# Performance work log

Hardware: AMD Instinct MI355X
Metric: run time of the kernel (lower is better)

The kernel has to match this reference:

```python
import jax, jax.numpy as jnp
import numpy as np

B, S, E, H, DK = 2, 2048, 2048, 16, 128


def _make_freq_pos_enc(dim, max_seq_len):
    # matches torch freq_pos_enc: interleaved repeat '(f r)' with r=2
    inv_freq = 1.0 / (10000.0 ** (jnp.arange(0, dim, 2, dtype=jnp.float32) / dim))
    pos = jnp.arange(max_seq_len, dtype=jnp.float32)
    pe = pos[:, None] * inv_freq[None, :]          # [S, dim/2]
    return jnp.repeat(pe, 2, axis=-1)              # [S, dim], interleaved


def setup_inputs() -> dict:
    key = jax.random.key(0)
    ks = jax.random.split(key, 5)
    sc = 1.0 / np.sqrt(E)
    return {
        "x": jax.random.normal(ks[0], (B, S, E), jnp.float32),
        "wq": jax.random.normal(ks[1], (H * DK, E), jnp.float32) * sc,
        "wk": jax.random.normal(ks[2], (H * DK, E), jnp.float32) * sc,
        "wv": jax.random.normal(ks[3], (H * DK, E), jnp.float32) * sc,
        "wo": jax.random.normal(ks[4], (E, H * DK), jnp.float32) * sc,
        "freq_pos_enc": _make_freq_pos_enc(DK, S),
        "num_heads": H,
        "d_k": DK,
    }


def rotate_half(u):
    # interleaved pairs: (d r) with r=2 -> (-u2, u1) interleaved back
    shp = u.shape
    u = u.reshape(shp[:-1] + (shp[-1] // 2, 2))
    u1, u2 = u[..., 0], u[..., 1]
    return jnp.stack((-u2, u1), axis=-1).reshape(shp)


def reference(x, wq, wk, wv, wo, freq_pos_enc, num_heads, d_k):
    b, s, _ = x.shape

    def proj(w):  # [B,S,E] @ [E, H*DK] -> [B,H,S,DK]
        return (x @ w.T).reshape(b, s, num_heads, d_k).transpose(0, 2, 1, 3)

    q, k, v = proj(wq), proj(wk), proj(wv)

    pe = freq_pos_enc[:s]                           # [S, DK]
    cos, sin = jnp.cos(pe), jnp.sin(pe)
    rot = lambda u: u * cos + rotate_half(u) * sin  # broadcast over [B,H]
    q, k = rot(q), rot(k)

    scale = 1.0 / jnp.sqrt(jnp.asarray(d_k, x.dtype))
    scores = jnp.einsum('bhqd,bhkd->bhqk', q, k) * scale
    causal = jnp.tril(jnp.ones((s, s), bool))
    scores = jnp.where(causal, scores, jnp.finfo(scores.dtype).min)
    attn = jnp.einsum('bhqk,bhkd->bhqd', jax.nn.softmax(scores, axis=-1), v)

    out = attn.transpose(0, 2, 1, 3).reshape(b, s, num_heads * d_k)
    return out @ wo.T
```

## Files before the change

kernel.cpp:

```cpp
#include <hip/hip_runtime.h>
#include <hip/hip_bf16.h>

typedef __attribute__((ext_vector_type(8))) short bf16x8;
typedef __attribute__((ext_vector_type(4))) float f32x4;
typedef unsigned short u16;
typedef unsigned int u32;

#define B_ 2
#define S_ 2048
#define E_ 2048
#define H_ 16
#define DK_ 128
#define SCALE_ 0.08838834764831845f
#define THR_RAW_ 90.5f

#define MFMA16(a,b,c) __builtin_amdgcn_mfma_f32_16x16x32_bf16((a),(b),(c),0,0,0)
#define GLD16(g, l) __builtin_amdgcn_global_load_lds((const __attribute__((address_space(1))) void*)(g), (__attribute__((address_space(3))) void*)(l), 16, 0, 0)

__device__ __forceinline__ float b2f(short s) {
    u32 u = ((u32)(u16)s) << 16;
    float f; __builtin_memcpy(&f, &u, 4); return f;
}

__global__ void cast_f32_bf16(const float* __restrict__ in, __hip_bfloat16* __restrict__ out, int n4) {
    int i = blockIdx.x * blockDim.x + threadIdx.x;
    if (i >= n4) return;
    float4 v = ((const float4*)in)[i];
    __hip_bfloat16 ob[4] = {__float2bfloat16(v.x), __float2bfloat16(v.y),
                            __float2bfloat16(v.z), __float2bfloat16(v.w)};
    ushort4 u; __builtin_memcpy(&u, ob, 8);
    ((ushort4*)out)[i] = u;
}

__global__ void cast_w4(const float* __restrict__ w0, const float* __restrict__ w1,
                        const float* __restrict__ w2, const float* __restrict__ w3,
                        __hip_bfloat16* __restrict__ o0, __hip_bfloat16* __restrict__ o1,
                        __hip_bfloat16* __restrict__ o2, __hip_bfloat16* __restrict__ o3,
                        int n4) {
    int i = blockIdx.x * blockDim.x + threadIdx.x;
    if (i >= n4) return;
    const float* in = blockIdx.y == 0 ? w0 : blockIdx.y == 1 ? w1 : blockIdx.y == 2 ? w2 : w3;
    __hip_bfloat16* out = blockIdx.y == 0 ? o0 : blockIdx.y == 1 ? o1 : blockIdx.y == 2 ? o2 : o3;
    float4 v = ((const float4*)in)[i];
    __hip_bfloat16 ob[4] = {__float2bfloat16(v.x), __float2bfloat16(v.y),
                            __float2bfloat16(v.z), __float2bfloat16(v.w)};
    ushort4 u; __builtin_memcpy(&u, ob, 8);
    ((ushort4*)out)[i] = u;
}

__global__ void trig_table(const float* __restrict__ pe, float* __restrict__ ct,
                           float* __restrict__ st) {
    int t = blockIdx.x * blockDim.x + threadIdx.x;
    int s = t >> 6, d2 = t & 63;
    float ang = pe[(size_t)s * DK_ + 2 * d2];
    ct[t] = cosf(ang);
    st[t] = sinf(ang);
}


#define ST_B(BUF, Q, KB) do { \
    int row_ = (Q) * 64 + (tid >> 3); \
    int gc_ = ((tid & 7) * 16) ^ ((row_ & 7) << 4); \
    GLD16(Wb + (size_t)(n0 + row_) * K2 + (KB) + gc_, (char*)Bs[BUF] + (Q) * 8192 + tid * 16); \
} while (0)

#define ST_A(BUF, Q, KB) do { \
    int row_ = (Q) * 64 + (tid >> 3); \
    int gc_ = ((tid & 7) * 16) ^ ((row_ & 7) << 4); \
    GLD16(Ab + (size_t)(m0 + row_) * K2 + (KB) + gc_, (char*)As[BUF] + (Q) * 8192 + tid * 16); \
} while (0)

#define WAIT_MFMA_ENTER() do { \
    __builtin_amdgcn_s_barrier(); \
    asm volatile("s_waitcnt lgkmcnt(0)" ::: "memory"); \
    __builtin_amdgcn_sched_barrier(0); \
    __builtin_amdgcn_s_setprio(1); \
} while (0)

__global__ __launch_bounds__(512, 2)
void gemm_qkv8(const __hip_bfloat16* __restrict__ X,
               const __hip_bfloat16* __restrict__ Wcat,
               __hip_bfloat16* __restrict__ Qo, __hip_bfloat16* __restrict__ Ko,
               __hip_bfloat16* __restrict__ Vo,
               const float* __restrict__ CT, const float* __restrict__ ST)
{
    __shared__ __align__(16) __hip_bfloat16 As[2][256 * 64];
    __shared__ __align__(16) __hip_bfloat16 Bs[2][192 * 64];
    const int tid = threadIdx.x, lane = tid & 63, wid = tid >> 6;
    const int wm = wid >> 2, wn = wid & 3;
    const int g = lane >> 4, c = lane & 15;
    const int raw = blockIdx.x;
    const int wg = (raw & 7) * 64 + (raw >> 3);
    const int mtile = wg & 15, ntile = wg >> 4;
    const int m0 = mtile * 256, n0 = ntile * 192;
    const long K2 = E_ * 2;
    const char* Ab = (const char*)X;
    const char* Wb = (const char*)Wcat;

    f32x4 acc[8][3];
    #pragma unroll
    for (int i = 0; i < 8; ++i)
        #pragma unroll
        for (int j = 0; j < 3; ++j) acc[i][j] = f32x4{0.f, 0.f, 0.f, 0.f};

    bf16x8 af[4][2], b01[2][2], b2[2];

    ST_B(0, 0, 0); ST_B(0, 1, 0); ST_B(0, 2, 0);
    ST_A(0, 0, 0); ST_A(0, 2, 0);
    ST_A(0, 1, 0); ST_A(0, 3, 0);
    asm volatile("s_waitcnt vmcnt(2)" ::: "memory");
    __builtin_amdgcn_s_barrier();

    #pragma unroll 1
    for (int t = 0; t < 32; ++t) {
        const int buf = t & 1;
        const long kb1 = (long)(t + 1) * 128;
        const char* Ac = (const char*)As[buf];
        const char* Bc = (const char*)Bs[buf];

        #pragma unroll
        for (int i = 0; i < 4; ++i) {
            int ar = wm * 128 + i * 16 + c;
            const char* ab = Ac + ar * 128;
            af[i][0] = *(const bf16x8*)(ab + ((g * 16) ^ ((ar & 7) << 4)));
            af[i][1] = *(const bf16x8*)(ab + ((64 + g * 16) ^ ((ar & 7) << 4)));
        }
        #pragma unroll
        for (int nj = 0; nj < 2; ++nj) {
            int br = wn * 48 + nj * 16 + c;
            const char* bb = Bc + br * 128;
            b01[nj][0] = *(const bf16x8*)(bb + ((g * 16) ^ ((br & 7) << 4)));
            b01[nj][1] = *(const bf16x8*)(bb + ((64 + g * 16) ^ ((br & 7) << 4)));
        }
        if (t < 31) { ST_B(buf ^ 1, 0, kb1); ST_B(buf ^ 1, 1, kb1); ST_B(buf ^ 1, 2, kb1); }
        WAIT_MFMA_ENTER();
        #pragma unroll
        for (int i = 0; i < 4; ++i)
            #pragma unroll
            for (int nj = 0; nj < 2; ++nj)
                #pragma unroll
                for (int k = 0; k < 2; ++k)
                    acc[i][nj] = MFMA16(af[i][k], b01[nj][k], acc[i][nj]);
        __builtin_amdgcn_s_setprio(0);
        __builtin_amdgcn_s_barrier();

        {
            int br = wn * 48 + 32 + c;
            const char* bb = Bc + br * 128;
            b2[0] = *(const bf16x8*)(bb + ((g * 16) ^ ((br & 7) << 4)));
            b2[1] = *(const bf16x8*)(bb + ((64 + g * 16) ^ ((br & 7) << 4)));
        }
        if (t < 31) { ST_A(buf ^ 1, 0, kb1); ST_A(buf ^ 1, 2, kb1); }
        WAIT_MFMA_ENTER();
        #pragma unroll
        for (int i = 0; i < 4; ++i)
            #pragma unroll
            for (int k = 0; k < 2; ++k)
                acc[i][2] = MFMA16(af[i][k], b2[k], acc[i][2]);
        __builtin_amdgcn_s_setprio(0);
        if (t < 31) { asm volatile("s_waitcnt vmcnt(5)" ::: "memory"); }
        else        { asm volatile("s_waitcnt vmcnt(0)" ::: "memory"); }
        __builtin_amdgcn_s_barrier();

        #pragma unroll
        for (int i = 0; i < 4; ++i) {
            int ar = wm * 128 + 64 + i * 16 + c;
            const char* ab = Ac + ar * 128;
            af[i][0] = *(const bf16x8*)(ab + ((g * 16) ^ ((ar & 7) << 4)));
            af[i][1] = *(const bf16x8*)(ab + ((64 + g * 16) ^ ((ar & 7) << 4)));
        }
        if (t < 31) { ST_A(buf ^ 1, 1, kb1); ST_A(buf ^ 1, 3, kb1); }
        WAIT_MFMA_ENTER();
        #pragma unroll
        for (int i = 0; i < 4; ++i)
            #pragma unroll
            for (int nj = 0; nj < 2; ++nj)
                #pragma unroll
                for (int k = 0; k < 2; ++k)
                    acc[4 + i][nj] = MFMA16(af[i][k], b01[nj][k], acc[4 + i][nj]);
        __builtin_amdgcn_s_setprio(0);
        __builtin_amdgcn_s_barrier();

        __builtin_amdgcn_s_setprio(1);
        #pragma unroll
        for (int i = 0; i < 4; ++i)
            #pragma unroll
            for (int k = 0; k < 2; ++k)
                acc[4 + i][2] = MFMA16(af[i][k], b2[k], acc[4 + i][2]);
        __builtin_amdgcn_s_setprio(0);
        if (t < 31) { asm volatile("s_waitcnt vmcnt(2)" ::: "memory"); }
        __builtin_amdgcn_s_barrier();
    }

    #pragma unroll
    for (int mi = 0; mi < 8; ++mi) {
        #pragma unroll
        for (int nj = 0; nj < 3; ++nj) {
            const int nbase = n0 + wn * 48 + nj * 16;
            const int t0 = nbase >> 11, t1 = (nbase + 15) >> 11;
            const int m_r0 = m0 + wm * 128 + mi * 16 + 4 * g;
            const int bb = m_r0 >> 11;
            if (t0 == 2 && t1 == 2) {
                const int n = nbase + c, d = n & (DK_ - 1), h = (n >> 7) & 15;
                const int s0 = m_r0 & (S_ - 1);
                __hip_bfloat16 ob[4];
                #pragma unroll
                for (int r = 0; r < 4; ++r) ob[r] = __float2bfloat16(acc[mi][nj][r]);
                ushort4 u; __builtin_memcpy(&u, ob, 8);
                size_t a = ((size_t)(bb * 16 + h) * DK_ + d) * S_ + s0;
                *(ushort4*)(Vo + a) = u;
            } else if (t1 < 2) {
                __hip_bfloat16* Cq = (t0 == 0) ? Qo : Ko;
                const int n = nbase + c, d = n & (DK_ - 1), h = (n >> 7) & 15;
                #pragma unroll
                for (int r = 0; r < 4; ++r) {
                    float v = acc[mi][nj][r];
                    float vp = __shfl_xor(v, 1);
                    int srow = (m_r0 + r) & (S_ - 1);
                    float cs = CT[srow * 64 + (d >> 1)];
                    float sn = ST[srow * 64 + (d >> 1)];
                    float o = (c & 1) ? __builtin_fmaf(v, cs, vp * sn)
                                      : __builtin_fmaf(v, cs, -vp * sn);
                    size_t a = ((size_t)(bb * 16 + h) * S_ + srow) * DK_ + d;
                    Cq[a] = __float2bfloat16(o);
                }
            } else {
                const int n = nbase + c, tens = n >> 11;
                const int rn = n & 2047, d = rn & (DK_ - 1), h = rn >> 7;
                #pragma unroll
                for (int r = 0; r < 4; ++r) {
                    float v = acc[mi][nj][r];
                    float vp = __shfl_xor(v, 1);
                    int srow = (m_r0 + r) & (S_ - 1);
                    if (tens == 2) {
                        size_t a = ((size_t)(bb * 16 + h) * DK_ + d) * S_ + srow;
                        Vo[a] = __float2bfloat16(v);
                    } else {
                        __hip_bfloat16* Cq = (tens == 0) ? Qo : Ko;
                        float cs = CT[srow * 64 + (d >> 1)];
                        float sn = ST[srow * 64 + (d >> 1)];
                        float o = (c & 1) ? __builtin_fmaf(v, cs, vp * sn)
                                          : __builtin_fmaf(v, cs, -vp * sn);
                        size_t a = ((size_t)(bb * 16 + h) * S_ + srow) * DK_ + d;
                        Cq[a] = __float2bfloat16(o);
                    }
                }
            }
        }
    }
}

__global__ __launch_bounds__(256, 2)
void gemm_out(const __hip_bfloat16* __restrict__ A, const __hip_bfloat16* __restrict__ W,
              float* __restrict__ Cout, int M, int N, int K)
{
    __shared__ __align__(16) __hip_bfloat16 As[128 * 64];
    __shared__ __align__(16) __hip_bfloat16 Bs[128 * 64];
    const int tid = threadIdx.x;
    const int lane = tid & 63, wv = tid >> 6;
    const int wr = wv >> 1, wc = wv & 1;
    const int m0 = blockIdx.x * 128, n0 = blockIdx.y * 128;
    const int g = lane >> 4, c = lane & 15;

    f32x4 acc[4][4];
    #pragma unroll
    for (int i = 0; i < 4; ++i)
        #pragma unroll
        for (int j = 0; j < 4; ++j) acc[i][j] = f32x4{0.f, 0.f, 0.f, 0.f};

    for (int k0 = 0; k0 < K; k0 += 64) {
        __syncthreads();
        #pragma unroll
        for (int it = 0; it < 4; ++it) {
            int o = (it * 256 + tid) * 16;
            int row = o >> 7;
            int colb = (o ^ ((row & 7) << 4)) & 127;
            GLD16((const char*)(A + (size_t)(m0 + row) * K + k0) + colb, (char*)As + o);
            GLD16((const char*)(W + (size_t)(n0 + row) * K + k0) + colb, (char*)Bs + o);
        }
        __syncthreads();
        #pragma unroll
        for (int ks = 0; ks < 2; ++ks) {
            bf16x8 af[4], bfm[4];
            #pragma unroll
            for (int i = 0; i < 4; ++i) {
                int arow = wr * 64 + i * 16 + c;
                int ab = arow * 128 + ((ks * 64 + g * 16) ^ ((arow & 7) << 4));
                af[i] = *(const bf16x8*)((const char*)As + ab);
                int brow = wc * 64 + i * 16 + c;
                int bb = brow * 128 + ((ks * 64 + g * 16) ^ ((brow & 7) << 4));
                bfm[i] = *(const bf16x8*)((const char*)Bs + bb);
            }
            #pragma unroll
            for (int i = 0; i < 4; ++i)
                #pragma unroll
                for (int j = 0; j < 4; ++j)
                    acc[i][j] = MFMA16(af[i], bfm[j], acc[i][j]);
        }
    }

    #pragma unroll
    for (int i = 0; i < 4; ++i)
        #pragma unroll
        for (int j = 0; j < 4; ++j)
            #pragma unroll
            for (int r = 0; r < 4; ++r) {
                int m = m0 + wr * 64 + i * 16 + 4 * g + r;
                int n = n0 + wc * 64 + j * 16 + c;
                Cout[(size_t)m * N + n] = acc[i][j][r];
            }
}

__device__ __forceinline__ void stage_kv(const __hip_bfloat16* Kp, const __hip_bfloat16* Vp,
                                         char* ks, char* vs, int kv0, int tid) {
    #pragma unroll
    for (int it = 0; it < 4; ++it) {
        int o = (it * 256 + tid) * 16;
        int row = o >> 8;
        int cb = (o ^ ((row & 7) << 4)) & 255;
        GLD16((const char*)(Kp + (size_t)(kv0 + row) * DK_) + cb, ks + o);
    }
    #pragma unroll
    for (int it = 0; it < 4; ++it) {
        int o = (it * 256 + tid) * 16;
        int row = o >> 7;
        int cb = (o ^ ((row & 7) << 4)) & 127;
        GLD16((const char*)(Vp + (size_t)row * S_ + kv0) + cb, vs + o);
    }
}

__global__ __launch_bounds__(256, 2)
void attn_kernel(const __hip_bfloat16* __restrict__ Q,
                 const __hip_bfloat16* __restrict__ Kt,
                 const __hip_bfloat16* __restrict__ VT,
                 __hip_bfloat16* __restrict__ O)
{
    __shared__ __align__(16) __hip_bfloat16 Ks[2][64 * 128];
    __shared__ __align__(16) __hip_bfloat16 Vs[2][128 * 64];
    __shared__ __align__(16) __hip_bfloat16 Ps[4][16 * 72];

    const int tid = threadIdx.x, lane = tid & 63, w = tid >> 6;
    const int g = lane >> 4, c = lane & 15;
    const int id = blockIdx.x;
    const int slot = id & 7, jj = id >> 3;
    const int bh = ((jj >> 4) << 3) | slot;
    const int xq = jj & 15;
    const int b = bh >> 4, h = bh & 15;
    const size_t base_bh = (size_t)bh * S_ * DK_;
    const __hip_bfloat16* Qp = Q + base_bh;
    const __hip_bfloat16* Kp = Kt + base_bh;
    const __hip_bfloat16* Vp = VT + base_bh;

    #pragma unroll 1
    for (int pass = 0; pass < 2; ++pass) {
        const int qt = pass ? (31 - xq) : xq;
        const int qw = qt * 64 + w * 16;
        const int ntiles = qt + 1;

        bf16x8 qf[4];
        #pragma unroll
        for (int ds = 0; ds < 4; ++ds)
            qf[ds] = *(const bf16x8*)(Qp + (size_t)(qw + c) * DK_ + ds * 32 + g * 8);

        f32x4 oacc[8];
        #pragma unroll
        for (int fd = 0; fd < 8; ++fd) oacc[fd] = f32x4{0.f, 0.f, 0.f, 0.f};
        float M[4], L[4];
        #pragma unroll
        for (int r = 0; r < 4; ++r) { M[r] = -1e30f; L[r] = 0.f; }

        stage_kv(Kp, Vp, (char*)Ks[0], (char*)Vs[0], 0, tid);
        __syncthreads();

        int cur = 0;
        for (int t = 0; t < ntiles; ++t) {
            const int kv0 = t * 64;
            if (t + 1 < ntiles)
                stage_kv(Kp, Vp, (char*)Ks[cur ^ 1], (char*)Vs[cur ^ 1], kv0 + 64, tid);

            const bool diag = (kv0 + 63 > qw);

            f32x4 sacc[4];
            #pragma unroll
            for (int f = 0; f < 4; ++f) sacc[f] = f32x4{0.f, 0.f, 0.f, 0.f};
            #pragma unroll
            for (int f = 0; f < 4; ++f) {
                #pragma unroll
                for (int ds = 0; ds < 4; ++ds) {
                    int krow = f * 16 + c;
                    int kbyt = krow * 256 + ((ds * 64 + g * 16) ^ ((krow & 7) << 4));
                    bf16x8 kf = *(const bf16x8*)((const char*)Ks[cur] + kbyt);
                    sacc[f] = MFMA16(qf[ds], kf, sacc[f]);
                }
            }

            float p[4][4];
            float mt[4] = {-1e30f, -1e30f, -1e30f, -1e30f};
            #pragma unroll
            for (int f = 0; f < 4; ++f)
                #pragma unroll
                for (int r = 0; r < 4; ++r) {
                    float v = sacc[f][r];
                    if (diag && (kv0 + f * 16 + c > qw + 4 * g + r)) v = -1e30f;
                    p[f][r] = v;
                    mt[r] = fmaxf(mt[r], v);
                }
            #pragma unroll
            for (int r = 0; r < 4; ++r) {
                float v = mt[r];
                v = fmaxf(v, __shfl_xor(v, 1));
                v = fmaxf(v, __shfl_xor(v, 2));
                v = fmaxf(v, __shfl_xor(v, 4));
                v = fmaxf(v, __shfl_xor(v, 8));
                mt[r] = v;
            }
            bool grow = (mt[0] > M[0] + THR_RAW_) || (mt[1] > M[1] + THR_RAW_) ||
                        (mt[2] > M[2] + THR_RAW_) || (mt[3] > M[3] + THR_RAW_);
            if (__any(grow)) {
                float al[4];
                #pragma unroll
                for (int r = 0; r < 4; ++r) {
                    float mn = fmaxf(M[r], mt[r]);
                    al[r] = __expf((M[r] - mn) * SCALE_);
                    M[r] = mn;
                    L[r] *= al[r];
                }
                #pragma unroll
                for (int fd = 0; fd < 8; ++fd)
                    #pragma unroll
                    for (int r = 0; r < 4; ++r) oacc[fd][r] *= al[r];
            }
            float ms[4];
            #pragma unroll
            for (int r = 0; r < 4; ++r) ms[r] = M[r] * SCALE_;
            float lt[4] = {0.f, 0.f, 0.f, 0.f};
            #pragma unroll
            for (int f = 0; f < 4; ++f)
                #pragma unroll
                for (int r = 0; r < 4; ++r) {
                    float e = __expf(__builtin_fmaf(p[f][r], SCALE_, -ms[r]));
                    lt[r] += e;
                    Ps[w][(4 * g + r) * 72 + f * 16 + c] = __float2bfloat16(e);
                }
            #pragma unroll
            for (int r = 0; r < 4; ++r) {
                float v = lt[r];
                v += __shfl_xor(v, 1);
                v += __shfl_xor(v, 2);
                v += __shfl_xor(v, 4);
                v += __shfl_xor(v, 8);
                L[r] += v;
            }

            #pragma unroll
            for (int ks2 = 0; ks2 < 2; ++ks2) {
                bf16x8 pf = *(const bf16x8*)&Ps[w][c * 72 + ks2 * 32 + g * 8];
                #pragma unroll
                for (int fd = 0; fd < 8; ++fd) {
                    int vrow = fd * 16 + c;
                    int vb = vrow * 128 + ((ks2 * 64 + g * 16) ^ ((vrow & 7) << 4));
                    bf16x8 vf = *(const bf16x8*)((const char*)Vs[cur] + vb);
                    oacc[fd] = MFMA16(pf, vf, oacc[fd]);
                }
            }
            __syncthreads();
            cur ^= 1;
        }

        float rl[4];
        #pragma unroll
        for (int r = 0; r < 4; ++r) rl[r] = 1.0f / L[r];
        #pragma unroll
        for (int fd = 0; fd < 8; ++fd) {
            #pragma unroll
            for (int r = 0; r < 4; ++r) {
                int s = qw + 4 * g + r;
                size_t a = ((size_t)(b * S_ + s)) * (H_ * DK_) + h * DK_ + fd * 16 + c;
                O[a] = __float2bfloat16(oacc[fd][r] * rl[r]);
            }
        }
    }
}

extern "C" void kernel_launch(void* const* d_in, const int* in_sizes, int n_in,
                              void* d_out, int out_size, void* d_ws, size_t ws_size,
                              hipStream_t stream) {
    const float* x  = (const float*)d_in[0];
    const float* wq = (const float*)d_in[1];
    const float* wk = (const float*)d_in[2];
    const float* wv = (const float*)d_in[3];
    const float* wo = (const float*)d_in[4];
    const float* pe = (const float*)d_in[5];
    float* out = (float*)d_out;

    const size_t XE = (size_t)B_ * S_ * E_;
    const size_t WE = (size_t)E_ * H_ * DK_;
    __hip_bfloat16* xb  = (__hip_bfloat16*)d_ws;
    __hip_bfloat16* wqb = xb + XE;
    __hip_bfloat16* wkb = wqb + WE;
    __hip_bfloat16* wvb = wkb + WE;
    __hip_bfloat16* wob = wvb + WE;
    __hip_bfloat16* qb  = wob + WE;
    __hip_bfloat16* kb  = qb + XE;
    __hip_bfloat16* vT  = kb + XE;
    __hip_bfloat16* at  = vT + XE;
    float* ct = (float*)(at + XE);
    float* st = ct + (size_t)S_ * 64;

    cast_f32_bf16<<<dim3((int)(XE / 4 / 256)), 256, 0, stream>>>(x, xb, (int)(XE / 4));
    cast_w4<<<dim3((int)(WE / 4 / 256), 4), 256, 0, stream>>>(wq, wk, wv, wo,
                                                              wqb, wkb, wvb, wob,
                                                              (int)(WE / 4));
    trig_table<<<dim3(S_ * 64 / 256), 256, 0, stream>>>(pe, ct, st);

    gemm_qkv8<<<dim3(512), 512, 0, stream>>>(xb, wqb, qb, kb, vT, ct, st);

    attn_kernel<<<dim3(512), 256, 0, stream>>>(qb, kb, vT, at);

    gemm_out<<<dim3(32, 16), 256, 0, stream>>>(at, wob, out, B_ * S_, E_, H_ * DK_);
}
```

Baseline: 267.6 us.

## Simplify QKV GEMM main loop to single-stage prefetch with two k-half MFMA passes

Replaces the hand-interleaved four-phase QKV GEMM loop with a simpler schedule. All next-tile A and B global-to-LDS loads are issued at the top of each iteration. Two k-half passes then each read 8 A and 3 B fragments and run 24 MFMAs, and one __syncthreads closes the iteration. This removes the split barriers and partial vmcnt waits, aiming for longer uninterrupted MFMA bursts and less barrier overhead. The cost is less fine-grained overlap of LDS reads with MFMA, more live fragment registers, and a full wait on outstanding loads at every iteration's barrier.

```diff
diff --git a/kernel.cpp b/kernel.cpp
--- a/kernel.cpp
+++ b/kernel.cpp
@@ -68,13 +68,6 @@
     int row_ = (Q) * 64 + (tid >> 3); \
     int gc_ = ((tid & 7) * 16) ^ ((row_ & 7) << 4); \
     GLD16(Ab + (size_t)(m0 + row_) * K2 + (KB) + gc_, (char*)As[BUF] + (Q) * 8192 + tid * 16); \
-} while (0)
-
-#define WAIT_MFMA_ENTER() do { \
-    __builtin_amdgcn_s_barrier(); \
-    asm volatile("s_waitcnt lgkmcnt(0)" ::: "memory"); \
-    __builtin_amdgcn_sched_barrier(0); \
-    __builtin_amdgcn_s_setprio(1); \
 } while (0)
 
 __global__ __launch_bounds__(512, 2)
@@ -103,13 +96,9 @@
         #pragma unroll
         for (int j = 0; j < 3; ++j) acc[i][j] = f32x4{0.f, 0.f, 0.f, 0.f};
 
-    bf16x8 af[4][2], b01[2][2], b2[2];
-
     ST_B(0, 0, 0); ST_B(0, 1, 0); ST_B(0, 2, 0);
-    ST_A(0, 0, 0); ST_A(0, 2, 0);
-    ST_A(0, 1, 0); ST_A(0, 3, 0);
-    asm volatile("s_waitcnt vmcnt(2)" ::: "memory");
-    __builtin_amdgcn_s_barrier();
+    ST_A(0, 0, 0); ST_A(0, 1, 0); ST_A(0, 2, 0); ST_A(0, 3, 0);
+    __syncthreads();
 
     #pragma unroll 1
     for (int t = 0; t < 32; ++t) {
@@ -118,78 +107,53 @@
         const char* Ac = (const char*)As[buf];
         const char* Bc = (const char*)Bs[buf];
 
-        #pragma unroll
-        for (int i = 0; i < 4; ++i) {
-            int ar = wm * 128 + i * 16 + c;
-            const char* ab = Ac + ar * 128;
-            af[i][0] = *(const bf16x8*)(ab + ((g * 16) ^ ((ar & 7) << 4)));
-            af[i][1] = *(const bf16x8*)(ab + ((64 + g * 16) ^ ((ar & 7) << 4)));
-        }
-        #pragma unroll
-        for (int nj = 0; nj < 2; ++nj) {
-            int br = wn * 48 + nj * 16 + c;
-            const char* bb = Bc + br * 128;
-            b01[nj][0] = *(const bf16x8*)(bb + ((g * 16) ^ ((br & 7) << 4)));
-            b01[nj][1] = *(const bf16x8*)(bb + ((64 + g * 16) ^ ((br & 7) << 4)));
-        }
-        if (t < 31) { ST_B(buf ^ 1, 0, kb1); ST_B(buf ^ 1, 1, kb1); ST_B(buf ^ 1, 2, kb1); }
-        WAIT_MFMA_ENTER();
-        #pragma unroll
-        for (int i = 0; i < 4; ++i)
-            #pragma unroll
-            for (int nj = 0; nj < 2; ++nj)
-                #pragma unroll
-                for (int k = 0; k < 2; ++k)
-                    acc[i][nj] = MFMA16(af[i][k], b01[nj][k], acc[i][nj]);
-        __builtin_amdgcn_s_setprio(0);
-        __builtin_amdgcn_s_barrier();
+        if (t < 31) {
+            ST_B(buf ^ 1, 0, kb1); ST_B(buf ^ 1, 1, kb1); ST_B(buf ^ 1, 2, kb1);
+            ST_A(buf ^ 1, 0, kb1); ST_A(buf ^ 1, 1, kb1); ST_A(buf ^ 1, 2, kb1); ST_A(buf ^ 1, 3, kb1);
+        }
 
         {
-            int br = wn * 48 + 32 + c;
-            const char* bb = Bc + br * 128;
-            b2[0] = *(const bf16x8*)(bb + ((g * 16) ^ ((br & 7) << 4)));
-            b2[1] = *(const bf16x8*)(bb + ((64 + g * 16) ^ ((br & 7) << 4)));
-        }
-        if (t < 31) { ST_A(buf ^ 1, 0, kb1); ST_A(buf ^ 1, 2, kb1); }
-        WAIT_MFMA_ENTER();
-        #pragma unroll
-        for (int i = 0; i < 4; ++i)
-            #pragma unroll
-            for (int k = 0; k < 2; ++k)
-                acc[i][2] = MFMA16(af[i][k], b2[k], acc[i][2]);
-        __builtin_amdgcn_s_setprio(0);
-        if (t < 31) { asm volatile("s_waitcnt vmcnt(5)" ::: "memory"); }
-        else        { asm volatile("s_waitcnt vmcnt(0)" ::: "memory"); }
-        __builtin_amdgcn_s_barrier();
-
-        #pragma unroll
-        for (int i = 0; i < 4; ++i) {
-            int ar = wm * 128 + 64 + i * 16 + c;
-            const char* ab = Ac + ar * 128;
-            af[i][0] = *(const bf16x8*)(ab + ((g * 16) ^ ((ar & 7) << 4)));
-            af[i][1] = *(const bf16x8*)(ab + ((64 + g * 16) ^ ((ar & 7) << 4)));
-        }
-        if (t < 31) { ST_A(buf ^ 1, 1, kb1); ST_A(buf ^ 1, 3, kb1); }
-        WAIT_MFMA_ENTER();
-        #pragma unroll
-        for (int i = 0; i < 4; ++i)
-            #pragma unroll
-            for (int nj = 0; nj < 2; ++nj)
-                #pragma unroll
-                for (int k = 0; k < 2; ++k)
-                    acc[4 + i][nj] = MFMA16(af[i][k], b01[nj][k], acc[4 + i][nj]);
-        __builtin_amdgcn_s_setprio(0);
-        __builtin_amdgcn_s_barrier();
-
-        __builtin_amdgcn_s_setprio(1);
-        #pragma unroll
-        for (int i = 0; i < 4; ++i)
-            #pragma unroll
-            for (int k = 0; k < 2; ++k)
-                acc[4 + i][2] = MFMA16(af[i][k], b2[k], acc[4 + i][2]);
-        __builtin_amdgcn_s_setprio(0);
-        if (t < 31) { asm volatile("s_waitcnt vmcnt(2)" ::: "memory"); }
-        __builtin_amdgcn_s_barrier();
+            bf16x8 af[8], bfm[3];
+            #pragma unroll
+            for (int i = 0; i < 8; ++i) {
+                int ar = wm * 128 + i * 16 + c;
+                af[i] = *(const bf16x8*)(Ac + ar * 128 + ((g * 16) ^ ((ar & 7) << 4)));
+            }
+            #pragma unroll
+            for (int j = 0; j < 3; ++j) {
+                int br = wn * 48 + j * 16 + c;
+                bfm[j] = *(const bf16x8*)(Bc + br * 128 + ((g * 16) ^ ((br & 7) << 4)));
+            }
+            __builtin_amdgcn_s_setprio(1);
+            #pragma unroll
+            for (int i = 0; i < 8; ++i)
+                #pragma unroll
+                for (int j = 0; j < 3; ++j)
+                    acc[i][j] = MFMA16(af[i], bfm[j], acc[i][j]);
+            __builtin_amdgcn_s_setprio(0);
+        }
+        {
+            bf16x8 af[8], bfm[3];
+            #pragma unroll
+            for (int i = 0; i < 8; ++i) {
+                int ar = wm * 128 + i * 16 + c;
+                af[i] = *(const bf16x8*)(Ac + ar * 128 + ((64 + g * 16) ^ ((ar & 7) << 4)));
+            }
+            #pragma unroll
+            for (int j = 0; j < 3; ++j) {
+                int br = wn * 48 + j * 16 + c;
+                bfm[j] = *(const bf16x8*)(Bc + br * 128 + ((64 + g * 16) ^ ((br & 7) << 4)));
+            }
+            __builtin_amdgcn_s_setprio(1);
+            #pragma unroll
+            for (int i = 0; i < 8; ++i)
+                #pragma unroll
+                for (int j = 0; j < 3; ++j)
+                    acc[i][j] = MFMA16(af[i], bfm[j], acc[i][j]);
+            __builtin_amdgcn_s_setprio(0);
+        }
+
+        __syncthreads();
     }
 
     #pragma unroll
```

After: 275.8 us. 3.1% more time.
